# Performance work log

Measured on AMD Instinct MI355X. Metric: run time of the kernel, lower is better.

Reference implementation:

```python
import jax, jax.numpy as jnp
import numpy as np

REG_MAX = 16


def _yolo_losses(cls_preds, reg_preds, targets):
    # targets: [B, N, 5] = (class_id, x1, y1, x2, y2); class_id < 0 -> invalid
    mask = targets[..., 0] >= 0.0                      # [B, N]
    cid = jnp.maximum(targets[..., 0], 0.0).astype(jnp.int32)
    x1, y1, x2, y2 = (targets[..., k] for k in (1, 2, 3, 4))
    cx = (x1 + x2) * 0.5
    cy = (y1 + y2) * 0.5
    nvalid = mask.astype(cls_preds[0].dtype).sum(-1)   # [B] valid targets per image
    cls_l = jnp.float32(0.0)
    box_l = jnp.float32(0.0)
    dfl_l = jnp.float32(0.0)
    for i, (cp, rp) in enumerate(zip(cls_preds, reg_preds)):
        B, nc, H, W = cp.shape
        s = 8.0 * (2 ** i)                             # stride of this FPN level
        # int() truncation == floor for positive coords, then clamp (as in torch)
        gx = jnp.clip((cx / s).astype(jnp.int32), 0, W - 1)   # [B, N]
        gy = jnp.clip((cy / s).astype(jnp.int32), 0, H - 1)
        # Faithful to torch's cls_pred_b.view(-1, nc): row r of the CE input is
        # the r-th contiguous nc-chunk of the flattened [C,H,W] tensor.
        logits = cp.reshape(B, H * W, nc)
        lse = jax.nn.logsumexp(logits, axis=-1)        # [B, HW]
        base = jnp.mean(lse - logits[..., 0], axis=-1) # CE when every row label is 0
        bi = jnp.arange(B)[:, None]
        t = gy * W + gx                                # row whose label becomes cid
        adj = (logits[bi, t, 0] - logits[bi, t, cid]) / (H * W)  # [B, N]
        # original recomputes full-grid CE once PER target -> n_valid * base + adj
        cls_l = cls_l + jnp.sum(base * nvalid) + jnp.sum(jnp.where(mask, adj, 0.0))
        pred = rp[bi, :, gy, gx].reshape(B, -1, 4, REG_MAX)      # [B, N, 4, reg_max]
        tx = (cx - gx.astype(cx.dtype) * s) / s
        ty = (cy - gy.astype(cy.dtype) * s) / s
        treg = jnp.stack([tx, ty, (x2 - x1) / s, (y2 - y1) / s], axis=-1)  # [B,N,4]
        box_per = jnp.mean(jnp.abs(pred.mean(-1) - treg), axis=-1)         # [B,N]
        dfl_per = jnp.mean(jnp.abs(pred - treg[..., None]), axis=(-2, -1)) # [B,N]
        box_l = box_l + jnp.sum(jnp.where(mask, box_per, 0.0))
        dfl_l = dfl_l + jnp.sum(jnp.where(mask, dfl_per, 0.0))
    total = 0.3 * cls_l + 8.0 * box_l + 1.5 * dfl_l
    return total, cls_l, box_l, dfl_l


def setup_inputs() -> dict:
    key = jax.random.key(0)
    B, N, NC, RM = 32, 64, 4, REG_MAX
    IMG = 1024.0
    ks = jax.random.split(key, 13)
    sizes = [128, 64, 32, 16]  # strides 8, 16, 32, 64 on a 1024px image
    inp = {}
    for j, hw in enumerate(sizes):
        inp[f"cls_p{j + 3}"] = jax.random.normal(ks[j], (B, NC, hw, hw), jnp.float32)
        inp[f"reg_p{j + 3}"] = jax.random.normal(ks[4 + j], (B, 4 * RM, hw, hw), jnp.float32)
    cx = jax.random.uniform(ks[8], (B, N), minval=64.0, maxval=IMG - 64.0)
    cy = jax.random.uniform(ks[9], (B, N), minval=64.0, maxval=IMG - 64.0)
    w = jax.random.uniform(ks[10], (B, N), minval=8.0, maxval=128.0)
    h = jax.random.uniform(ks[11], (B, N), minval=8.0, maxval=128.0)
    cid = jax.random.randint(ks[12], (B, N), 0, NC).astype(jnp.float32)
    inp["targets"] = jnp.stack(
        [cid, cx - w / 2, cy - h / 2, cx + w / 2, cy + h / 2], axis=-1
    )
    return inp


def reference(cls_p3, cls_p4, cls_p5, cls_p6, reg_p3, reg_p4, reg_p5, reg_p6, targets):
    cls_preds = [cls_p3, cls_p4, cls_p5, cls_p6]
    reg_preds = [reg_p3, reg_p4, reg_p5, reg_p6]
    total, cls_l, box_l, dfl_l = _yolo_losses(cls_preds, reg_preds, targets)
    return total, cls_l, box_l, dfl_l
```

## Files before the change

### kernel.cpp

```cpp
#include <hip/hip_runtime.h>
#include <math.h>


__device__ inline float waveReduceSum(float v) {
#pragma unroll
    for (int m = 32; m >= 1; m >>= 1) v += __shfl_xor(v, m, 64);
    return v;
}

__global__ __launch_bounds__(256) void target_kernel(
    const float* __restrict__ c0, const float* __restrict__ c1,
    const float* __restrict__ c2, const float* __restrict__ c3,
    const float* __restrict__ r0, const float* __restrict__ r1,
    const float* __restrict__ r2, const float* __restrict__ r3,
    const float* __restrict__ tgt, float* __restrict__ ws)
{
    int tid = blockIdx.x * 256 + threadIdx.x;
    int lvl = tid >> 11;
    int b   = (tid >> 6) & 31;
    int n   = tid & 63;

    const float* T = tgt + (b * 64 + n) * 5;
    float t0 = T[0], x1 = T[1], y1 = T[2], x2 = T[3], y2 = T[4];
    bool mask = t0 >= 0.f;

    unsigned long long bal = __ballot(mask);
    if (lvl == 0 && (threadIdx.x & 63) == 0) ws[b] = (float)__popcll(bal);

    float cx = (x1 + x2) * 0.5f, cy = (y1 + y2) * 0.5f;
    int Wl = 128 >> lvl;
    int HW = Wl * Wl;
    float s = (float)(8 << lvl);
    float invs = 1.f / s;
    int gx = (int)(cx * invs); gx = min(max(gx, 0), Wl - 1);
    int gy = (int)(cy * invs); gy = min(max(gy, 0), Wl - 1);
    int cid = (int)fmaxf(t0, 0.f); cid = min(max(cid, 0), 3);

    const float* cp; const float* rp;
    if (lvl == 0)      { cp = c0; rp = r0; }
    else if (lvl == 1) { cp = c1; rp = r1; }
    else if (lvl == 2) { cp = c2; rp = r2; }
    else               { cp = c3; rp = r3; }

    int t = gy * Wl + gx;
    const float* cb = cp + ((size_t)b * 4 * HW + 4 * t);
    float adj = (cb[0] - cb[cid]) / (float)HW;

    const float* rb = rp + ((size_t)b * 64 * HW + t);
    float tx = (cx - (float)gx * s) * invs;
    float ty = (cy - (float)gy * s) * invs;
    float treg[4] = { tx, ty, (x2 - x1) * invs, (y2 - y1) * invs };

    float boxsum = 0.f, dflsum = 0.f;
#pragma unroll
    for (int d = 0; d < 4; ++d) {
        float tr = treg[d];
        float s16 = 0.f;
#pragma unroll
        for (int m = 0; m < 16; ++m) {
            float v = rb[(size_t)(d * 16 + m) * HW];
            s16 += v;
            dflsum += fabsf(v - tr);
        }
        boxsum += fabsf(s16 * (1.f / 16.f) - tr);
    }
    float box_per = boxsum * 0.25f;
    float dfl_per = dflsum * (1.f / 64.f);
    if (!mask) { adj = 0.f; box_per = 0.f; dfl_per = 0.f; }

    __shared__ float red[4][3];
    float wa = waveReduceSum(adj);
    float wb = waveReduceSum(box_per);
    float wd = waveReduceSum(dfl_per);
    int lane = threadIdx.x & 63, wid = threadIdx.x >> 6;
    if (lane == 0) { red[wid][0] = wa; red[wid][1] = wb; red[wid][2] = wd; }
    __syncthreads();
    if (threadIdx.x == 0) {
        atomicAdd(&ws[33], red[0][0] + red[1][0] + red[2][0] + red[3][0]);
        atomicAdd(&ws[34], red[0][1] + red[1][1] + red[2][1] + red[3][1]);
        atomicAdd(&ws[35], red[0][2] + red[1][2] + red[2][2] + red[3][2]);
    }
}

__global__ __launch_bounds__(256) void base_kernel(
    const float* __restrict__ c0, const float* __restrict__ c1,
    const float* __restrict__ c2, const float* __restrict__ c3,
    const float* __restrict__ nvalid, float* __restrict__ partials)
{
    constexpr int E0 = 32 * 16384;
    constexpr int E1 = E0 + 32 * 4096;
    constexpr int E2 = E1 + 32 * 1024;
    constexpr int E3 = E2 + 32 * 256;

    float acc = 0.f;
    int stride = gridDim.x * 256;
    for (int c = blockIdx.x * 256 + threadIdx.x; c < E3; c += stride) {
        const float* p; int local; int lg; float invHW;
        if (c < E0)      { p = c0; local = c;      lg = 14; invHW = 1.f / 16384.f; }
        else if (c < E1) { p = c1; local = c - E0; lg = 12; invHW = 1.f / 4096.f; }
        else if (c < E2) { p = c2; local = c - E1; lg = 10; invHW = 1.f / 1024.f; }
        else             { p = c3; local = c - E2; lg = 8;  invHW = 1.f / 256.f; }
        float4 v = ((const float4*)p)[local];
        float mx = fmaxf(fmaxf(v.x, v.y), fmaxf(v.z, v.w));
        float lse = logf(expf(v.x - mx) + expf(v.y - mx) +
                         expf(v.z - mx) + expf(v.w - mx)) + mx;
        acc += (lse - v.x) * nvalid[local >> lg] * invHW;
    }

    float w = waveReduceSum(acc);
    __shared__ float red[4];
    int lane = threadIdx.x & 63, wid = threadIdx.x >> 6;
    if (lane == 0) red[wid] = w;
    __syncthreads();
    if (threadIdx.x == 0)
        partials[blockIdx.x] = red[0] + red[1] + red[2] + red[3];
}

__global__ __launch_bounds__(256) void finalize_kernel(
    const float* __restrict__ ws, const float* __restrict__ partials,
    int np, float* __restrict__ out)
{
    float acc = 0.f;
    for (int i = threadIdx.x; i < np; i += 256) acc += partials[i];
    float w = waveReduceSum(acc);
    __shared__ float red[4];
    int lane = threadIdx.x & 63, wid = threadIdx.x >> 6;
    if (lane == 0) red[wid] = w;
    __syncthreads();
    if (threadIdx.x == 0) {
        float base = red[0] + red[1] + red[2] + red[3];
        float cls = base + ws[33];
        float box = ws[34];
        float dfl = ws[35];
        out[0] = 0.3f * cls + 8.f * box + 1.5f * dfl;
        out[1] = cls;
        out[2] = box;
        out[3] = dfl;
    }
}

extern "C" void kernel_launch(void* const* d_in, const int* in_sizes, int n_in,
                              void* d_out, int out_size, void* d_ws, size_t ws_size,
                              hipStream_t stream) {
    const float* c0 = (const float*)d_in[0];
    const float* r0 = (const float*)d_in[1];
    const float* c1 = (const float*)d_in[2];
    const float* r1 = (const float*)d_in[3];
    const float* c2 = (const float*)d_in[4];
    const float* r2 = (const float*)d_in[5];
    const float* c3 = (const float*)d_in[6];
    const float* r3 = (const float*)d_in[7];
    const float* tgt = (const float*)d_in[8];
    float* ws = (float*)d_ws;
    float* out = (float*)d_out;

    constexpr int K1_BLOCKS = 1024;

    hipMemsetAsync(d_ws, 0, 36 * sizeof(float), stream);
    target_kernel<<<32, 256, 0, stream>>>(c0, c1, c2, c3, r0, r1, r2, r3, tgt, ws);
    base_kernel<<<K1_BLOCKS, 256, 0, stream>>>(c0, c1, c2, c3, ws, ws + 36);
    finalize_kernel<<<1, 256, 0, stream>>>(ws, ws + 36, K1_BLOCKS, out);
}
```

Baseline: 249.9 us.

## Spread per-target regression gather across 16 threads and 512 blocks

Restructures the target kernel so each target's 64 regression values are loaded by 16 threads (4 per box side), with shuffle reductions for the per-side mean. The grid grows from 32 to 512 blocks, exposing far more memory-level parallelism for the strided gathers. The valid-count per image moves from a ballot write to an atomic accumulation, which adds some atomics.

Result: faster. 236.5 us (-5.4%).

```diff
diff --git a/kernel.cpp b/kernel.cpp
--- a/kernel.cpp
+++ b/kernel.cpp
@@ -15,17 +15,20 @@
     const float* __restrict__ r2, const float* __restrict__ r3,
     const float* __restrict__ tgt, float* __restrict__ ws)
 {
-    int tid = blockIdx.x * 256 + threadIdx.x;
-    int lvl = tid >> 11;
-    int b   = (tid >> 6) & 31;
-    int n   = tid & 63;
+    int lvl = blockIdx.x >> 7;
+    int rem = blockIdx.x & 127;
+    int b   = rem >> 2;
+    int g   = rem & 3;
+
+    int tid = threadIdx.x;
+    int n_local = tid >> 4;
+    int d = (tid >> 2) & 3;
+    int q = tid & 3;
+    int n = g * 16 + n_local;
 
     const float* T = tgt + (b * 64 + n) * 5;
     float t0 = T[0], x1 = T[1], y1 = T[2], x2 = T[3], y2 = T[4];
     bool mask = t0 >= 0.f;
-
-    unsigned long long bal = __ballot(mask);
-    if (lvl == 0 && (threadIdx.x & 63) == 0) ws[b] = (float)__popcll(bal);
 
     float cx = (x1 + x2) * 0.5f, cy = (y1 + y2) * 0.5f;
     int Wl = 128 >> lvl;
@@ -43,42 +46,51 @@
     else               { cp = c3; rp = r3; }
 
     int t = gy * Wl + gx;
-    const float* cb = cp + ((size_t)b * 4 * HW + 4 * t);
-    float adj = (cb[0] - cb[cid]) / (float)HW;
+
+    float tx = (cx - (float)gx * s) * invs;
+    float ty = (cy - (float)gy * s) * invs;
+    float tr = (d == 0) ? tx : (d == 1) ? ty
+             : (d == 2) ? (x2 - x1) * invs : (y2 - y1) * invs;
 
     const float* rb = rp + ((size_t)b * 64 * HW + t);
-    float tx = (cx - (float)gx * s) * invs;
-    float ty = (cy - (float)gy * s) * invs;
-    float treg[4] = { tx, ty, (x2 - x1) * invs, (y2 - y1) * invs };
+    float v0 = rb[(size_t)(d * 16 + q * 4 + 0) * HW];
+    float v1 = rb[(size_t)(d * 16 + q * 4 + 1) * HW];
+    float v2 = rb[(size_t)(d * 16 + q * 4 + 2) * HW];
+    float v3 = rb[(size_t)(d * 16 + q * 4 + 3) * HW];
 
-    float boxsum = 0.f, dflsum = 0.f;
-#pragma unroll
-    for (int d = 0; d < 4; ++d) {
-        float tr = treg[d];
-        float s16 = 0.f;
-#pragma unroll
-        for (int m = 0; m < 16; ++m) {
-            float v = rb[(size_t)(d * 16 + m) * HW];
-            s16 += v;
-            dflsum += fabsf(v - tr);
+    float s4 = v0 + v1 + v2 + v3;
+    float dfl_c = fabsf(v0 - tr) + fabsf(v1 - tr) +
+                  fabsf(v2 - tr) + fabsf(v3 - tr);
+    float s8  = s4 + __shfl_xor(s4, 1, 64);
+    float s16 = s8 + __shfl_xor(s8, 2, 64);
+
+    float box_c = 0.f, adj_c = 0.f, nv_c = 0.f;
+    if (q == 0) {
+        box_c = fabsf(s16 * (1.f / 16.f) - tr) * 0.25f;
+        if (d == 0) {
+            const float* cb = cp + ((size_t)b * 4 * HW + 4 * t);
+            adj_c = (cb[0] - cb[cid]) / (float)HW;
+            nv_c = mask ? 1.f : 0.f;
         }
-        boxsum += fabsf(s16 * (1.f / 16.f) - tr);
     }
-    float box_per = boxsum * 0.25f;
-    float dfl_per = dflsum * (1.f / 64.f);
-    if (!mask) { adj = 0.f; box_per = 0.f; dfl_per = 0.f; }
+    if (!mask) { adj_c = 0.f; box_c = 0.f; dfl_c = 0.f; }
+    dfl_c *= (1.f / 64.f);
 
-    __shared__ float red[4][3];
-    float wa = waveReduceSum(adj);
-    float wb = waveReduceSum(box_per);
-    float wd = waveReduceSum(dfl_per);
-    int lane = threadIdx.x & 63, wid = threadIdx.x >> 6;
-    if (lane == 0) { red[wid][0] = wa; red[wid][1] = wb; red[wid][2] = wd; }
+    float ra = waveReduceSum(adj_c);
+    float rbx = waveReduceSum(box_c);
+    float rd = waveReduceSum(dfl_c);
+    float rn = waveReduceSum(nv_c);
+    __shared__ float red[4][4];
+    int lane = tid & 63, wid = tid >> 6;
+    if (lane == 0) { red[wid][0] = ra; red[wid][1] = rbx;
+                     red[wid][2] = rd; red[wid][3] = rn; }
     __syncthreads();
-    if (threadIdx.x == 0) {
+    if (tid == 0) {
         atomicAdd(&ws[33], red[0][0] + red[1][0] + red[2][0] + red[3][0]);
         atomicAdd(&ws[34], red[0][1] + red[1][1] + red[2][1] + red[3][1]);
         atomicAdd(&ws[35], red[0][2] + red[1][2] + red[2][2] + red[3][2]);
+        if (lvl == 0)
+            atomicAdd(&ws[b], red[0][3] + red[1][3] + red[2][3] + red[3][3]);
     }
 }
 
@@ -157,7 +169,7 @@
     constexpr int K1_BLOCKS = 1024;
 
     hipMemsetAsync(d_ws, 0, 36 * sizeof(float), stream);
-    target_kernel<<<32, 256, 0, stream>>>(c0, c1, c2, c3, r0, r1, r2, r3, tgt, ws);
+    target_kernel<<<512, 256, 0, stream>>>(c0, c1, c2, c3, r0, r1, r2, r3, tgt, ws);
     base_kernel<<<K1_BLOCKS, 256, 0, stream>>>(c0, c1, c2, c3, ws, ws + 36);
     finalize_kernel<<<1, 256, 0, stream>>>(ws, ws + 36, K1_BLOCKS, out);
 }
```
